# Kernel tuning notes

Measured on AMD Instinct MI355X. Metric: run time of the kernel, lower is better.

## Reference

```python
import jax, jax.numpy as jnp
import numpy as np

B = 8192
D = 512          # hidden_dim
OBS_EMB = 256
COMM = 128
N_ACT = 4
N_LAYERS = 2
D_INNER = 2 * D
D_STATE = 16
DT_RANK = D // 16  # 32
D_CONV = 4
EPS = 1e-5


def _xavier(k, shape):
    s = jnp.sqrt(2.0 / (shape[-2] + shape[-1]))
    return jax.random.normal(k, shape, jnp.float32) * s


def setup_inputs() -> dict:
    ks = jax.random.split(jax.random.key(0), 16)
    p = {}
    p['obs'] = jax.random.normal(ks[0], (B, 75), jnp.float32)
    p['comm_in'] = jax.random.normal(ks[1], (B, COMM), jnp.float32)
    # obs encoder: Conv2d(3->32, k=3, valid) + Linear(288->256)
    p['conv_w'] = jax.random.normal(ks[2], (32, 3, 3, 3), jnp.float32) * jnp.sqrt(2.0 / 27.0)
    p['conv_b'] = jnp.zeros((32,), jnp.float32)
    p['enc_w'] = _xavier(ks[3], (288, OBS_EMB))
    p['enc_b'] = jnp.zeros((OBS_EMB,), jnp.float32)
    p['proj_w'] = _xavier(ks[4], (OBS_EMB + COMM, D))
    p['proj_b'] = jnp.zeros((D,), jnp.float32)
    # Mamba stack params (stacked over layers)
    p['norm_w'] = jnp.ones((N_LAYERS, D), jnp.float32)
    p['in_proj_w'] = _xavier(ks[5], (N_LAYERS, D, 2 * D_INNER))
    p['conv1d_w'] = jax.random.normal(ks[6], (N_LAYERS, D_INNER, D_CONV), jnp.float32) / jnp.sqrt(D_CONV)
    p['conv1d_b'] = jnp.zeros((N_LAYERS, D_INNER), jnp.float32)
    p['x_proj_w'] = _xavier(ks[7], (N_LAYERS, D_INNER, DT_RANK + 2 * D_STATE))
    p['dt_proj_w'] = _xavier(ks[8], (N_LAYERS, DT_RANK, D_INNER))
    p['dt_proj_b'] = jnp.full((N_LAYERS, D_INNER), jnp.log(jnp.expm1(0.01)), jnp.float32)  # dt ~ 0.01
    p['A_log'] = jnp.log(jnp.broadcast_to(jnp.arange(1, D_STATE + 1, dtype=jnp.float32), (N_LAYERS, D_INNER, D_STATE)))
    p['D_param'] = jnp.ones((N_LAYERS, D_INNER), jnp.float32)
    p['out_proj_w'] = _xavier(ks[9], (N_LAYERS, D_INNER, D))
    p['final_norm_w'] = jnp.ones((D,), jnp.float32)
    # output heads
    p['act_w'] = _xavier(ks[10], (D, N_ACT)); p['act_b'] = jnp.zeros((N_ACT,), jnp.float32)
    p['comm_w'] = _xavier(ks[11], (D, COMM)); p['comm_b'] = jnp.zeros((COMM,), jnp.float32)
    p['val_w'] = _xavier(ks[12], (D, 1)); p['val_b'] = jnp.zeros((1,), jnp.float32)
    return p


def _rmsnorm(x, w):
    return x * jax.lax.rsqrt(jnp.mean(x * x, axis=-1, keepdims=True) + EPS) * w


def _mamba_block(u, Wi, cw, cb, Wx, Wdt, bdt, Alog, Dp, Wo):
    # u: (B, L, D) -> (B, L, D)
    Bsz, L, _ = u.shape
    d_inner = Dp.shape[0]
    x, z = jnp.split(u @ Wi, 2, axis=-1)                       # (B,L,di) each
    # causal depthwise conv1d over L
    xt = jnp.pad(jnp.swapaxes(x, 1, 2), ((0, 0), (0, 0), (D_CONV - 1, 0)))
    xc = jax.lax.conv_general_dilated(xt, cw[:, None, :], (1,), 'VALID',
                                      feature_group_count=d_inner,
                                      dimension_numbers=('NCH', 'OIH', 'NCH'))
    x = jax.nn.silu(jnp.swapaxes(xc, 1, 2) + cb)
    x_dbl = x @ Wx                                              # (B,L,dt_rank+2*ns)
    dt = jax.nn.softplus(x_dbl[..., :DT_RANK] @ Wdt + bdt)      # (B,L,di)
    Bm = x_dbl[..., DT_RANK:DT_RANK + D_STATE]                  # (B,L,ns)
    Cm = x_dbl[..., DT_RANK + D_STATE:]                         # (B,L,ns)
    A = -jnp.exp(Alog)                                          # (di,ns)
    dA = jnp.exp(dt[..., None] * A)                             # (B,L,di,ns)
    dBx = dt[..., None] * Bm[:, :, None, :] * x[..., None]      # (B,L,di,ns)

    def step(h, inp):
        dA_t, dBx_t, C_t = inp
        h = dA_t * h + dBx_t
        return h, jnp.einsum('bds,bs->bd', h, C_t)

    h0 = jnp.zeros((Bsz, d_inner, D_STATE), u.dtype)
    _, ys = jax.lax.scan(step, h0, (jnp.swapaxes(dA, 0, 1), jnp.swapaxes(dBx, 0, 1), jnp.swapaxes(Cm, 0, 1)))
    y = jnp.swapaxes(ys, 0, 1) + x * Dp
    return (y * jax.nn.silu(z)) @ Wo


def reference(obs, comm_in, conv_w, conv_b, enc_w, enc_b, proj_w, proj_b,
              norm_w, in_proj_w, conv1d_w, conv1d_b, x_proj_w, dt_proj_w, dt_proj_b,
              A_log, D_param, out_proj_w, final_norm_w,
              act_w, act_b, comm_w, comm_b, val_w, val_b):
    Bsz = obs.shape[0]
    v = obs.reshape(Bsz, 3, 5, 5)
    v = jax.lax.conv_general_dilated(v, conv_w, (1, 1), 'VALID',
                                     dimension_numbers=('NCHW', 'OIHW', 'NCHW'))
    v = jax.nn.relu(v + conv_b[None, :, None, None]).reshape(Bsz, -1)   # (B,288)
    emb = jax.nn.relu(v @ enc_w + enc_b)                                 # (B,256)
    x = jax.nn.relu(jnp.concatenate([emb, comm_in], axis=-1) @ proj_w + proj_b)  # (B,512)
    h = x[:, None, :]                                                    # (B, L=1, D)
    for i in range(norm_w.shape[0]):
        h = h + _mamba_block(_rmsnorm(h, norm_w[i]), in_proj_w[i], conv1d_w[i],
                             conv1d_b[i], x_proj_w[i], dt_proj_w[i], dt_proj_b[i],
                             A_log[i], D_param[i], out_proj_w[i])
    h = _rmsnorm(h, final_norm_w)[:, 0, :]
    action_logits = h @ act_w + act_b
    comm_out = jnp.tanh(h @ comm_w + comm_b)
    value = h @ val_w + val_b
    return action_logits, comm_out, value
```

## Files before the change

kernel.cpp:

```cpp
#include <hip/hip_runtime.h>
#include <math.h>


typedef __bf16 bf16x8 __attribute__((ext_vector_type(8)));
typedef float f32x4 __attribute__((ext_vector_type(4)));
typedef short short8 __attribute__((ext_vector_type(8)));

__device__ __forceinline__ float siluf(float v){ return v / (1.f + __expf(-v)); }
__device__ __forceinline__ float spfast(float v){ return v > 15.f ? v : __logf(1.f + __expf(v)); }
__device__ __forceinline__ float b2f(unsigned short u){ return __uint_as_float(((unsigned)u)<<16); }
__device__ __forceinline__ unsigned short f2b(float f){
  unsigned u = __float_as_uint(f);
  return (unsigned short)((u + 0x7fffu + ((u>>16)&1u)) >> 16);
}
__device__ __forceinline__ void g2l16(const void* g, void* l){
  __builtin_amdgcn_global_load_lds((const __attribute__((address_space(1))) unsigned int*)g,
                                   (__attribute__((address_space(3))) unsigned int*)l, 16, 0, 0);
}

__global__ __launch_bounds__(256) void k_wt_all(
    const float* __restrict__ in_proj_w, const float* __restrict__ out_proj_w,
    const float* __restrict__ x_proj_w,  const float* __restrict__ dt_proj_w,
    const float* __restrict__ enc_w,     const float* __restrict__ proj_w,
    const float* __restrict__ act_w, const float* __restrict__ comm_w, const float* __restrict__ val_w,
    const float* __restrict__ obs, const float* __restrict__ comm_in,
    const float* __restrict__ conv_w, const float* __restrict__ conv_b,
    unsigned short* __restrict__ wi_t, unsigned short* __restrict__ wo_t,
    unsigned short* __restrict__ wx_t, unsigned short* __restrict__ wdt_t,
    unsigned short* __restrict__ we_t, unsigned short* __restrict__ wp_t,
    unsigned short* __restrict__ wh_t,
    unsigned short* __restrict__ v, unsigned short* __restrict__ cat)
{
  int b = blockIdx.x;
  const int t = threadIdx.x;

  if (b >= 3792) {
    __shared__ float s_obs[8][76];
    const int r0 = (b - 3792) * 8;
    for (int i = t; i < 8*75; i += 256) s_obs[i/75][i%75] = obs[(size_t)(r0 + i/75)*75 + i%75];
    __syncthreads();
    for (int i = t; i < 8*288; i += 256) {
      int r = i / 288, o = i % 288;
      int c = o / 9, ij = o % 9, oi = ij/3, oj = ij%3;
      float acc = conv_b[c];
      #pragma unroll
      for (int ic=0; ic<3; ic++)
        #pragma unroll
        for (int ki=0; ki<3; ki++)
          #pragma unroll
          for (int kj=0; kj<3; kj++)
            acc = fmaf(s_obs[r][ic*25 + (oi+ki)*5 + (oj+kj)], conv_w[((c*3+ic)*3+ki)*3+kj], acc);
      v[(size_t)(r0+r)*320 + o] = f2b(fmaxf(acc, 0.f));
    }
    v[(size_t)(r0 + (t>>5))*320 + 288 + (t&31)] = 0;
    for (int i = t; i < 8*128; i += 256) {
      int r = i >> 7, c = i & 127;
      cat[(size_t)(r0+r)*384 + 256 + c] = f2b(comm_in[(size_t)(r0+r)*128 + c]);
    }
    return;
  }
  if (b >= 3536) {
    const int n = b - 3536;
    for (int k = t; k < 512; k += 256) {
      float v2;
      if (n < 4)         v2 = act_w[k*4 + n];
      else if (n < 132)  v2 = comm_w[k*128 + (n-4)];
      else if (n == 132) v2 = val_w[k];
      else               v2 = 0.f;
      wh_t[(size_t)n*512 + k] = f2b(v2);
    }
    return;
  }
  const float* Wsrc; unsigned short* Wdst; int Kd, Nd, KP, nkb;
  if (b < 2048) {
    const int L = b >> 10; b &= 1023;
    Wsrc = in_proj_w + (size_t)L*512*2048; Wdst = wi_t + (size_t)L*2048*512;
    Kd = 512; Nd = 2048; KP = 512; nkb = 16;
  } else if (b < 3072) {
    b -= 2048; const int L = b >> 9; b &= 511;
    Wsrc = out_proj_w + (size_t)L*1024*512; Wdst = wo_t + (size_t)L*512*1024;
    Kd = 1024; Nd = 512; KP = 1024; nkb = 32;
  } else if (b < 3200) {
    b -= 3072; const int L = b >> 6; b &= 63;
    Wsrc = x_proj_w + (size_t)L*1024*64; Wdst = wx_t + (size_t)L*64*1024;
    Kd = 1024; Nd = 64; KP = 1024; nkb = 32;
  } else if (b < 3264) {
    b -= 3200; const int L = b >> 5; b &= 31;
    Wsrc = dt_proj_w + (size_t)L*32*1024; Wdst = wdt_t + (size_t)L*1024*32;
    Kd = 32; Nd = 1024; KP = 32; nkb = 1;
  } else if (b < 3344) {
    b -= 3264; Wsrc = enc_w; Wdst = we_t; Kd = 288; Nd = 256; KP = 320; nkb = 10;
  } else {
    b -= 3344; Wsrc = proj_w; Wdst = wp_t; Kd = 384; Nd = 512; KP = 384; nkb = 12;
  }
  __shared__ float s[32][33];
  const int kb = (b % nkb)*32, nb = (b / nkb)*32;
  const int c = t & 31, r = t >> 5;
  #pragma unroll
  for (int i=0;i<32;i+=8) {
    const int k = kb + r + i;
    s[r+i][c] = (k < Kd) ? Wsrc[(size_t)k*Nd + nb + c] : 0.f;
  }
  __syncthreads();
  #pragma unroll
  for (int i=0;i<32;i+=8) Wdst[(size_t)(nb+r+i)*KP + kb + c] = f2b(s[c][r+i]);
}

__global__ __launch_bounds__(256) void k_rms(const float* __restrict__ h,
                                             const float* __restrict__ nw,
                                             unsigned short* __restrict__ u)
{
  const int l = threadIdx.x & 63;
  const size_t row = (size_t)blockIdx.x*4 + (threadIdx.x>>6);
  const float4* hp = (const float4*)(h + row*512) + l*2;
  float4 v0 = hp[0], v1 = hp[1];
  float ss = v0.x*v0.x+v0.y*v0.y+v0.z*v0.z+v0.w*v0.w
           + v1.x*v1.x+v1.y*v1.y+v1.z*v1.z+v1.w*v1.w;
  #pragma unroll
  for (int m=32;m;m>>=1) ss += __shfl_xor(ss, m, 64);
  const float sc = rsqrtf(ss*(1.f/512.f) + 1e-5f);
  const float4* np = (const float4*)nw + l*2;
  float4 w0 = np[0], w1 = np[1];
  short8 o;
  o[0]=(short)f2b(v0.x*sc*w0.x); o[1]=(short)f2b(v0.y*sc*w0.y);
  o[2]=(short)f2b(v0.z*sc*w0.z); o[3]=(short)f2b(v0.w*sc*w0.w);
  o[4]=(short)f2b(v1.x*sc*w1.x); o[5]=(short)f2b(v1.y*sc*w1.y);
  o[6]=(short)f2b(v1.z*sc*w1.z); o[7]=(short)f2b(v1.w*sc*w1.w);
  *(short8*)(u + row*512 + l*8) = o;
}

template<int K, int NB>
__device__ __forceinline__ void gemmT(const unsigned short* __restrict__ A,
                                      const unsigned short* __restrict__ Bt,
                                      int r0, int c0,
                                      unsigned short* sA, unsigned short* sB,
                                      f32x4 (&acc)[4][NB/32])
{
  constexpr int NF = NB/32;
  constexpr int ABUF = 128*64, BBUF = NB*64;
  const int tid = threadIdx.x;
  const int l = tid & 63;
  const int wr = (tid>>7)&1, wc = (tid>>6)&1;
  const int rowA = tid>>3, kc8 = (tid&7)*8;
  const unsigned short* gA = A  + (size_t)(r0+rowA)*K + kc8;
  const unsigned short* gB = Bt + (size_t)(c0+rowA)*K + kc8;
  const int aOff = (wr*64 + (l&15))*64 + ((l>>4)*8);
  const int bOff = (wc*(NB/2) + (l&15))*64 + ((l>>4)*8);

  auto stage = [&](int kt, int buf) {
    #pragma unroll
    for (int it=0; it<4; ++it)
      g2l16(gA + (size_t)(it*32)*K + kt, sA + buf*ABUF + (it*256+tid)*8);
    #pragma unroll
    for (int it=0; it<NF; ++it)
      g2l16(gB + (size_t)(it*32)*K + kt, sB + buf*BBUF + (it*256+tid)*8);
  };

  stage(0, 0);
  __syncthreads();
  int cur = 0;
  for (int kt=0; kt<K; kt+=64) {
    if (kt + 64 < K) stage(kt + 64, cur ^ 1);
    const unsigned short* pA = sA + cur*ABUF;
    const unsigned short* pB = sB + cur*BBUF;
    #pragma unroll
    for (int ks=0; ks<64; ks+=32) {
      bf16x8 af[4], bfm[NF];
      #pragma unroll
      for (int m=0;m<4;m++) af[m]  = *(const bf16x8*)(pA + (m*16)*64 + aOff + ks);
      #pragma unroll
      for (int n=0;n<NF;n++) bfm[n] = *(const bf16x8*)(pB + (n*16)*64 + bOff + ks);
      #pragma unroll
      for (int m=0;m<4;m++)
        #pragma unroll
        for (int n=0;n<NF;n++)
          acc[m][n] = __builtin_amdgcn_mfma_f32_16x16x32_bf16(af[m], bfm[n], acc[m][n], 0, 0, 0);
    }
    __syncthreads();
    cur ^= 1;
  }
}

__global__ __launch_bounds__(256) void k_gemm_inproj(
    const unsigned short* __restrict__ A, const unsigned short* __restrict__ Bt,
    const float* __restrict__ cw, const float* __restrict__ cb,
    unsigned short* __restrict__ xs, unsigned short* __restrict__ zs)
{
  __shared__ unsigned short sA[2*128*64], sB[2*128*64];
  f32x4 acc[4][4];
  #pragma unroll
  for (int m=0;m<4;m++)
    #pragma unroll
    for (int n=0;n<4;n++) acc[m][n] = (f32x4){0.f,0.f,0.f,0.f};
  const int r0 = blockIdx.x*128, c0 = blockIdx.y*128;
  gemmT<512,128>(A, Bt, r0, c0, sA, sB, acc);

  const int tid = threadIdx.x, l = tid & 63;
  const int wr = (tid>>7)&1, wc = (tid>>6)&1;
  const int colB = c0 + wc*64 + (l&15);
  const int rowB = r0 + wr*64 + ((l>>4)*4);
  if (c0 < 1024) {
    #pragma unroll
    for (int n=0;n<4;n++){
      const int col = colB + n*16;
      const float cw3 = cw[col*4+3], cbv = cb[col];
      #pragma unroll
      for (int m=0;m<4;m++)
        #pragma unroll
        for (int j=0;j<4;j++){
          const int row = rowB + m*16 + j;
          xs[(size_t)row*1024 + col] = f2b(siluf(fmaf(acc[m][n][j], cw3, cbv)));
        }
    }
  } else {
    #pragma unroll
    for (int n=0;n<4;n++){
      const int col = colB + n*16 - 1024;
      #pragma unroll
      for (int m=0;m<4;m++)
        #pragma unroll
        for (int j=0;j<4;j++){
          const int row = rowB + m*16 + j;
          zs[(size_t)row*1024 + col] = f2b(siluf(acc[m][n][j]));
        }
    }
  }
}

__global__ __launch_bounds__(256) void k_gemm_outproj(
    const unsigned short* __restrict__ A, const unsigned short* __restrict__ Bt,
    float* __restrict__ h)
{
  __shared__ unsigned short sA[2*128*64], sB[2*64*64];
  f32x4 acc[4][2];
  #pragma unroll
  for (int m=0;m<4;m++)
    #pragma unroll
    for (int n=0;n<2;n++) acc[m][n] = (f32x4){0.f,0.f,0.f,0.f};
  const int r0 = blockIdx.x*128, c0 = blockIdx.y*64;
  gemmT<1024,64>(A, Bt, r0, c0, sA, sB, acc);

  const int tid = threadIdx.x, l = tid & 63;
  const int wr = (tid>>7)&1, wc = (tid>>6)&1;
  const int colB = c0 + wc*32 + (l&15);
  const int rowB = r0 + wr*64 + ((l>>4)*4);
  #pragma unroll
  for (int n=0;n<2;n++){
    const int col = colB + n*16;
    #pragma unroll
    for (int m=0;m<4;m++)
      #pragma unroll
      for (int j=0;j<4;j++){
        const int row = rowB + m*16 + j;
        h[(size_t)row*512 + col] += acc[m][n][j];
      }
  }
}

__global__ __launch_bounds__(256) void k_gemm_enc(
    const unsigned short* __restrict__ A, const unsigned short* __restrict__ Bt,
    const float* __restrict__ bias, unsigned short* __restrict__ cat)
{
  __shared__ unsigned short sA[2*128*64], sB[2*64*64];
  f32x4 acc[4][2];
  #pragma unroll
  for (int m=0;m<4;m++)
    #pragma unroll
    for (int n=0;n<2;n++) acc[m][n] = (f32x4){0.f,0.f,0.f,0.f};
  const int r0 = blockIdx.x*128, c0 = blockIdx.y*64;
  gemmT<320,64>(A, Bt, r0, c0, sA, sB, acc);

  const int tid = threadIdx.x, l = tid & 63;
  const int wr = (tid>>7)&1, wc = (tid>>6)&1;
  const int colB = c0 + wc*32 + (l&15);
  const int rowB = r0 + wr*64 + ((l>>4)*4);
  #pragma unroll
  for (int n=0;n<2;n++){
    const int col = colB + n*16;
    const float bv = bias[col];
    #pragma unroll
    for (int m=0;m<4;m++)
      #pragma unroll
      for (int j=0;j<4;j++){
        const size_t row = rowB + m*16 + j;
        cat[row*384 + col] = f2b(fmaxf(acc[m][n][j] + bv, 0.f));
      }
  }
}

__global__ __launch_bounds__(256) void k_gemm_proj(
    const unsigned short* __restrict__ A, const unsigned short* __restrict__ Bt,
    const float* __restrict__ bias, float* __restrict__ h)
{
  __shared__ unsigned short sA[2*128*64], sB[2*64*64];
  f32x4 acc[4][2];
  #pragma unroll
  for (int m=0;m<4;m++)
    #pragma unroll
    for (int n=0;n<2;n++) acc[m][n] = (f32x4){0.f,0.f,0.f,0.f};
  const int r0 = blockIdx.x*128, c0 = blockIdx.y*64;
  gemmT<384,64>(A, Bt, r0, c0, sA, sB, acc);

  const int tid = threadIdx.x, l = tid & 63;
  const int wr = (tid>>7)&1, wc = (tid>>6)&1;
  const int colB = c0 + wc*32 + (l&15);
  const int rowB = r0 + wr*64 + ((l>>4)*4);
  #pragma unroll
  for (int n=0;n<2;n++){
    const int col = colB + n*16;
    const float bv = bias[col];
    #pragma unroll
    for (int m=0;m<4;m++)
      #pragma unroll
      for (int j=0;j<4;j++){
        const size_t row = rowB + m*16 + j;
        h[row*512 + col] = fmaxf(acc[m][n][j] + bv, 0.f);
      }
  }
}

__global__ __launch_bounds__(256) void k_gemm_heads(
    const unsigned short* __restrict__ A, const unsigned short* __restrict__ Bt,
    const float* __restrict__ act_b, const float* __restrict__ comm_b,
    const float* __restrict__ val_b, float* __restrict__ out)
{
  __shared__ unsigned short sA[2*128*64], sB[2*64*64];
  f32x4 acc[4][2];
  #pragma unroll
  for (int m=0;m<4;m++)
    #pragma unroll
    for (int n=0;n<2;n++) acc[m][n] = (f32x4){0.f,0.f,0.f,0.f};
  const int r0 = blockIdx.x*128, c0 = blockIdx.y*64;
  gemmT<512,64>(A, Bt, r0, c0, sA, sB, acc);

  const int tid = threadIdx.x, l = tid & 63;
  const int wr = (tid>>7)&1, wc = (tid>>6)&1;
  const int colB = c0 + wc*32 + (l&15);
  const int rowB = r0 + wr*64 + ((l>>4)*4);
  #pragma unroll
  for (int n=0;n<2;n++){
    const int col = colB + n*16;
    if (col > 132) continue;
    #pragma unroll
    for (int m=0;m<4;m++)
      #pragma unroll
      for (int j=0;j<4;j++){
        const size_t row = rowB + m*16 + j;
        float v = acc[m][n][j];
        if (col < 4)        out[row*4 + col] = v + act_b[col];
        else if (col < 132) out[32768 + row*128 + (col-4)] = tanhf(v + comm_b[col-4]);
        else                out[1081344 + row] = v + val_b[0];
      }
  }
}

__global__ __launch_bounds__(256) void k_ssm_f(
    unsigned short* __restrict__ xs, const unsigned short* __restrict__ zs,
    const unsigned short* __restrict__ Wx_t, const unsigned short* __restrict__ Wdt_t,
    const float* __restrict__ bdt, const float* __restrict__ Dp)
{
  __shared__ unsigned short sX[32*1024];
  __shared__ unsigned short sB[2*64*128];
  __shared__ float s_dbl[32][64];
  __shared__ unsigned short sDt[32*32];
  __shared__ float s_bc[32];
  constexpr int BB = 64*128;
  const int tid = threadIdx.x, l = tid & 63, w = tid >> 6;
  const int r0 = blockIdx.x * 32;

  auto stageWx = [&](int kt, int buf) {
    #pragma unroll
    for (int it=0; it<4; ++it) {
      const int idx = it*256 + tid;
      g2l16(Wx_t + (size_t)(idx>>4)*1024 + (idx&15)*8 + kt, sB + buf*BB + idx*8);
    }
  };

  #pragma unroll
  for (int it=0; it<16; ++it) {
    const int idx = it*256 + tid;
    g2l16(xs + (size_t)(r0 + (idx>>7))*1024 + (idx&127)*8, sX + idx*8);
  }
  stageWx(0, 0);
  __syncthreads();

  f32x4 acc0 = (f32x4){0.f,0.f,0.f,0.f}, acc1 = (f32x4){0.f,0.f,0.f,0.f};
  int cur = 0;
  for (int kt = 0; kt < 1024; kt += 128) {
    if (kt + 128 < 1024) stageWx(kt + 128, cur ^ 1);
    const unsigned short* pB = sB + cur*BB;
    #pragma unroll
    for (int ks=0; ks<128; ks+=32) {
      bf16x8 a0 = *(const bf16x8*)(sX + ((l&15))*1024    + (l>>4)*8 + kt + ks);
      bf16x8 a1 = *(const bf16x8*)(sX + (16+(l&15))*1024 + (l>>4)*8 + kt + ks);
      bf16x8 bf = *(const bf16x8*)(pB + (w*16+(l&15))*128 + (l>>4)*8 + ks);
      acc0 = __builtin_amdgcn_mfma_f32_16x16x32_bf16(a0, bf, acc0, 0, 0, 0);
      acc1 = __builtin_amdgcn_mfma_f32_16x16x32_bf16(a1, bf, acc1, 0, 0, 0);
    }
    __syncthreads();
    cur ^= 1;
  }

  auto stageWdt = [&](int c, int buf) {
    const int cc = c*256;
    #pragma unroll
    for (int it=0; it<4; ++it) {
      const int idx = it*256 + tid;
      g2l16(Wdt_t + (size_t)(cc + (idx>>2))*32 + (idx&3)*8, sB + buf*BB + idx*8);
    }
  };
  stageWdt(0, 0);

  #pragma unroll
  for (int j=0;j<4;j++) {
    s_dbl[(l>>4)*4 + j]     [w*16 + (l&15)] = acc0[j];
    s_dbl[16 + (l>>4)*4 + j][w*16 + (l&15)] = acc1[j];
  }
  __syncthreads();
  if (tid < 32) {
    float a = 0.f;
    #pragma unroll
    for (int s=0;s<16;s++) a = fmaf(s_dbl[tid][32+s], s_dbl[tid][48+s], a);
    s_bc[tid] = a;
  }
  {
    const int r = tid >> 3, c4 = (tid & 7)*4;
    sDt[r*32 + c4]   = f2b(s_dbl[r][c4]);
    sDt[r*32 + c4+1] = f2b(s_dbl[r][c4+1]);
    sDt[r*32 + c4+2] = f2b(s_dbl[r][c4+2]);
    sDt[r*32 + c4+3] = f2b(s_dbl[r][c4+3]);
  }
  __syncthreads();

  bf16x8 af0 = *(const bf16x8*)(sDt + ((l&15))*32    + (l>>4)*8);
  bf16x8 af1 = *(const bf16x8*)(sDt + (16+(l&15))*32 + (l>>4)*8);
  for (int c = 0; c < 4; ++c) {
    if (c + 1 < 4) stageWdt(c + 1, (c + 1) & 1);
    const unsigned short* pB = sB + (c & 1)*BB;
    f32x4 a2[2][4];
    #pragma unroll
    for (int n=0;n<4;n++){
      bf16x8 bn = *(const bf16x8*)(pB + (w*64 + n*16 + (l&15))*32 + (l>>4)*8);
      a2[0][n] = __builtin_amdgcn_mfma_f32_16x16x32_bf16(af0, bn, (f32x4){0.f,0.f,0.f,0.f}, 0, 0, 0);
      a2[1][n] = __builtin_amdgcn_mfma_f32_16x16x32_bf16(af1, bn, (f32x4){0.f,0.f,0.f,0.f}, 0, 0, 0);
    }
    const int cc = c*256;
    #pragma unroll
    for (int n=0;n<4;n++){
      const int col = cc + w*64 + n*16 + (l&15);
      const float bj = bdt[col], dpj = Dp[col];
      #pragma unroll
      for (int m=0;m<2;m++){
        #pragma unroll
        for (int j=0;j<4;j++){
          const int rloc = m*16 + (l>>4)*4 + j;
          const size_t row = r0 + rloc;
          const float dtv = spfast(a2[m][n][j] + bj);
          const float f = fmaf(dtv, s_bc[rloc], dpj);
          const float x = b2f(sX[rloc*1024 + col]);
          const float z = b2f(zs[row*1024 + col]);
          xs[row*1024 + col] = f2b(x * f * z);
        }
      }
    }
    __syncthreads();
  }
}

extern "C" void kernel_launch(void* const* d_in, const int* in_sizes, int n_in,
                              void* d_out, int out_size, void* d_ws, size_t ws_size,
                              hipStream_t stream) {
  const float* obs       = (const float*)d_in[0];
  const float* comm_in   = (const float*)d_in[1];
  const float* conv_w    = (const float*)d_in[2];
  const float* conv_b    = (const float*)d_in[3];
  const float* enc_w     = (const float*)d_in[4];
  const float* enc_b     = (const float*)d_in[5];
  const float* proj_w    = (const float*)d_in[6];
  const float* proj_b    = (const float*)d_in[7];
  const float* norm_w    = (const float*)d_in[8];
  const float* in_proj_w = (const float*)d_in[9];
  const float* conv1d_w  = (const float*)d_in[10];
  const float* conv1d_b  = (const float*)d_in[11];
  const float* x_proj_w  = (const float*)d_in[12];
  const float* dt_proj_w = (const float*)d_in[13];
  const float* dt_proj_b = (const float*)d_in[14];
  const float* D_param   = (const float*)d_in[16];
  const float* out_proj_w= (const float*)d_in[17];
  const float* final_nw  = (const float*)d_in[18];
  const float* act_w     = (const float*)d_in[19];
  const float* act_b     = (const float*)d_in[20];
  const float* comm_w    = (const float*)d_in[21];
  const float* comm_b    = (const float*)d_in[22];
  const float* val_w     = (const float*)d_in[23];
  const float* val_b     = (const float*)d_in[24];
  float* out = (float*)d_out;

  char* W = (char*)d_ws;
  float* h             = (float*)W;
  unsigned short* u_b  = (unsigned short*)(W + (16u<<20));
  unsigned short* xs_b = (unsigned short*)(W + (24u<<20));
  unsigned short* zs_b = (unsigned short*)(W + (40u<<20));
  unsigned short* wi_t = (unsigned short*)(W + (56u<<20));
  unsigned short* wo_t = (unsigned short*)(W + (60u<<20));
  unsigned short* wx_t = (unsigned short*)(W + (64u<<20));
  unsigned short* wdt_t= (unsigned short*)(W + (64u<<20) + (256u<<10));
  unsigned short* wh_t = (unsigned short*)(W + (65u<<20));
  unsigned short* we_t = (unsigned short*)(W + (65u<<20) + (512u<<10));
  unsigned short* wp_t = (unsigned short*)(W + (66u<<20));

  unsigned short* v_b   = xs_b;
  unsigned short* cat_b = zs_b;

  k_wt_all<<<4816,256,0,stream>>>(in_proj_w, out_proj_w, x_proj_w, dt_proj_w,
                                  enc_w, proj_w, act_w, comm_w, val_w,
                                  obs, comm_in, conv_w, conv_b,
                                  wi_t, wo_t, wx_t, wdt_t, we_t, wp_t, wh_t,
                                  v_b, cat_b);

  k_gemm_enc<<<dim3(64,4),256,0,stream>>>(v_b, we_t, enc_b, cat_b);
  k_gemm_proj<<<dim3(64,8),256,0,stream>>>(cat_b, wp_t, proj_b, h);

  for (int L=0; L<2; L++) {
    k_rms<<<2048,256,0,stream>>>(h, norm_w + L*512, u_b);
    k_gemm_inproj<<<dim3(64,16),256,0,stream>>>(u_b, wi_t + (size_t)L*2048*512,
                                                conv1d_w + L*1024*4, conv1d_b + L*1024, xs_b, zs_b);
    k_ssm_f<<<256,256,0,stream>>>(xs_b, zs_b, wx_t + (size_t)L*64*1024,
                                  wdt_t + (size_t)L*1024*32,
                                  dt_proj_b + L*1024, D_param + L*1024);
    k_gemm_outproj<<<dim3(64,8),256,0,stream>>>(xs_b, wo_t + (size_t)L*512*1024, h);
  }
  k_rms<<<2048,256,0,stream>>>(h, final_nw, u_b);
  k_gemm_heads<<<dim3(64,4),256,0,stream>>>(u_b, wh_t, act_b, comm_b, val_b, out);
}
```

Baseline: 235.2 us.

## Fuse RMSNorm into GEMM epilogues via row sum-of-squares and weight folding

Removes the three separate RMSNorm kernels. The norm weights are folded into the transposed in_proj and head weights. The producing GEMMs (proj, out_proj) now write a bf16 copy of h and accumulate per-row sums of squares through shared and global atomics, and the consuming GEMMs apply the rsqrt row scale in their epilogue. This saves a full read of h and a write of the normalized activations per norm, at the cost of atomics, extra zeroing blocks, and bf16 rounding of the unnormalized h before scaling.

```diff
diff --git a/kernel.cpp b/kernel.cpp
--- a/kernel.cpp
+++ b/kernel.cpp
@@ -17,23 +17,34 @@
   __builtin_amdgcn_global_load_lds((const __attribute__((address_space(1))) unsigned int*)g,
                                    (__attribute__((address_space(3))) unsigned int*)l, 16, 0, 0);
 }
+__device__ __forceinline__ float rowscale(const float* ssb, int row){
+  return rsqrtf(ssb[row]*(1.f/512.f) + 1e-5f);
+}
 
 __global__ __launch_bounds__(256) void k_wt_all(
     const float* __restrict__ in_proj_w, const float* __restrict__ out_proj_w,
     const float* __restrict__ x_proj_w,  const float* __restrict__ dt_proj_w,
     const float* __restrict__ enc_w,     const float* __restrict__ proj_w,
     const float* __restrict__ act_w, const float* __restrict__ comm_w, const float* __restrict__ val_w,
+    const float* __restrict__ norm_w, const float* __restrict__ final_nw,
     const float* __restrict__ obs, const float* __restrict__ comm_in,
     const float* __restrict__ conv_w, const float* __restrict__ conv_b,
     unsigned short* __restrict__ wi_t, unsigned short* __restrict__ wo_t,
     unsigned short* __restrict__ wx_t, unsigned short* __restrict__ wdt_t,
     unsigned short* __restrict__ we_t, unsigned short* __restrict__ wp_t,
     unsigned short* __restrict__ wh_t,
-    unsigned short* __restrict__ v, unsigned short* __restrict__ cat)
+    unsigned short* __restrict__ v, unsigned short* __restrict__ cat,
+    float* __restrict__ ssbufs )
 {
   int b = blockIdx.x;
   const int t = threadIdx.x;
 
+  if (b >= 4816) {
+    float4* p = (float4*)(ssbufs + (size_t)(b - 4816)*8192);
+    #pragma unroll
+    for (int i=0;i<8;i++) p[t + i*256] = (float4){0.f,0.f,0.f,0.f};
+    return;
+  }
   if (b >= 3792) {
     __shared__ float s_obs[8][76];
     const int r0 = (b - 3792) * 8;
@@ -67,15 +78,17 @@
       else if (n < 132)  v2 = comm_w[k*128 + (n-4)];
       else if (n == 132) v2 = val_w[k];
       else               v2 = 0.f;
-      wh_t[(size_t)n*512 + k] = f2b(v2);
+      wh_t[(size_t)n*512 + k] = f2b(v2 * final_nw[k]);
     }
     return;
   }
   const float* Wsrc; unsigned short* Wdst; int Kd, Nd, KP, nkb;
+  const float* nwf = nullptr;
   if (b < 2048) {
     const int L = b >> 10; b &= 1023;
     Wsrc = in_proj_w + (size_t)L*512*2048; Wdst = wi_t + (size_t)L*2048*512;
     Kd = 512; Nd = 2048; KP = 512; nkb = 16;
+    nwf = norm_w + L*512;
   } else if (b < 3072) {
     b -= 2048; const int L = b >> 9; b &= 511;
     Wsrc = out_proj_w + (size_t)L*1024*512; Wdst = wo_t + (size_t)L*512*1024;
@@ -102,31 +115,9 @@
     s[r+i][c] = (k < Kd) ? Wsrc[(size_t)k*Nd + nb + c] : 0.f;
   }
   __syncthreads();
-  #pragma unroll
-  for (int i=0;i<32;i+=8) Wdst[(size_t)(nb+r+i)*KP + kb + c] = f2b(s[c][r+i]);
-}
-
-__global__ __launch_bounds__(256) void k_rms(const float* __restrict__ h,
-                                             const float* __restrict__ nw,
-                                             unsigned short* __restrict__ u)
-{
-  const int l = threadIdx.x & 63;
-  const size_t row = (size_t)blockIdx.x*4 + (threadIdx.x>>6);
-  const float4* hp = (const float4*)(h + row*512) + l*2;
-  float4 v0 = hp[0], v1 = hp[1];
-  float ss = v0.x*v0.x+v0.y*v0.y+v0.z*v0.z+v0.w*v0.w
-           + v1.x*v1.x+v1.y*v1.y+v1.z*v1.z+v1.w*v1.w;
-  #pragma unroll
-  for (int m=32;m;m>>=1) ss += __shfl_xor(ss, m, 64);
-  const float sc = rsqrtf(ss*(1.f/512.f) + 1e-5f);
-  const float4* np = (const float4*)nw + l*2;
-  float4 w0 = np[0], w1 = np[1];
-  short8 o;
-  o[0]=(short)f2b(v0.x*sc*w0.x); o[1]=(short)f2b(v0.y*sc*w0.y);
-  o[2]=(short)f2b(v0.z*sc*w0.z); o[3]=(short)f2b(v0.w*sc*w0.w);
-  o[4]=(short)f2b(v1.x*sc*w1.x); o[5]=(short)f2b(v1.y*sc*w1.y);
-  o[6]=(short)f2b(v1.z*sc*w1.z); o[7]=(short)f2b(v1.w*sc*w1.w);
-  *(short8*)(u + row*512 + l*8) = o;
+  const float nwv = nwf ? nwf[kb + c] : 1.f;
+  #pragma unroll
+  for (int i=0;i<32;i+=8) Wdst[(size_t)(nb+r+i)*KP + kb + c] = f2b(s[c][r+i] * nwv);
 }
 
 template<int K, int NB>
@@ -183,6 +174,7 @@
 
 __global__ __launch_bounds__(256) void k_gemm_inproj(
     const unsigned short* __restrict__ A, const unsigned short* __restrict__ Bt,
+    const float* __restrict__ ssb,
     const float* __restrict__ cw, const float* __restrict__ cb,
     unsigned short* __restrict__ xs, unsigned short* __restrict__ zs)
 {
@@ -199,6 +191,11 @@
   const int wr = (tid>>7)&1, wc = (tid>>6)&1;
   const int colB = c0 + wc*64 + (l&15);
   const int rowB = r0 + wr*64 + ((l>>4)*4);
+  float sv[4][4];
+  #pragma unroll
+  for (int m=0;m<4;m++)
+    #pragma unroll
+    for (int j=0;j<4;j++) sv[m][j] = rowscale(ssb, rowB + m*16 + j);
   if (c0 < 1024) {
     #pragma unroll
     for (int n=0;n<4;n++){
@@ -209,7 +206,7 @@
         #pragma unroll
         for (int j=0;j<4;j++){
           const int row = rowB + m*16 + j;
-          xs[(size_t)row*1024 + col] = f2b(siluf(fmaf(acc[m][n][j], cw3, cbv)));
+          xs[(size_t)row*1024 + col] = f2b(siluf(fmaf(acc[m][n][j]*sv[m][j], cw3, cbv)));
         }
     }
   } else {
@@ -221,7 +218,7 @@
         #pragma unroll
         for (int j=0;j<4;j++){
           const int row = rowB + m*16 + j;
-          zs[(size_t)row*1024 + col] = f2b(siluf(acc[m][n][j]));
+          zs[(size_t)row*1024 + col] = f2b(siluf(acc[m][n][j]*sv[m][j]));
         }
     }
   }
@@ -229,9 +226,10 @@
 
 __global__ __launch_bounds__(256) void k_gemm_outproj(
     const unsigned short* __restrict__ A, const unsigned short* __restrict__ Bt,
-    float* __restrict__ h)
+    float* __restrict__ h, unsigned short* __restrict__ hb, float* __restrict__ ssb)
 {
   __shared__ unsigned short sA[2*128*64], sB[2*64*64];
+  __shared__ float s_ss[128];
   f32x4 acc[4][2];
   #pragma unroll
   for (int m=0;m<4;m++)
@@ -239,6 +237,45 @@
     for (int n=0;n<2;n++) acc[m][n] = (f32x4){0.f,0.f,0.f,0.f};
   const int r0 = blockIdx.x*128, c0 = blockIdx.y*64;
   gemmT<1024,64>(A, Bt, r0, c0, sA, sB, acc);
+
+  const int tid = threadIdx.x, l = tid & 63;
+  if (tid < 128) s_ss[tid] = 0.f;
+  __syncthreads();
+  const int wr = (tid>>7)&1, wc = (tid>>6)&1;
+  const int colB = c0 + wc*32 + (l&15);
+  const int rowB = r0 + wr*64 + ((l>>4)*4);
+  #pragma unroll
+  for (int m=0;m<4;m++)
+    #pragma unroll
+    for (int j=0;j<4;j++){
+      const int row = rowB + m*16 + j;
+      float c2 = 0.f;
+      #pragma unroll
+      for (int n=0;n<2;n++){
+        const int col = colB + n*16;
+        float hv = h[(size_t)row*512 + col] + acc[m][n][j];
+        h[(size_t)row*512 + col] = hv;
+        hb[(size_t)row*512 + col] = f2b(hv);
+        c2 = fmaf(hv, hv, c2);
+      }
+      atomicAdd(&s_ss[wr*64 + m*16 + ((l>>4)*4) + j], c2);
+    }
+  __syncthreads();
+  if (tid < 128) atomicAdd(&ssb[r0 + tid], s_ss[tid]);
+}
+
+__global__ __launch_bounds__(256) void k_gemm_enc(
+    const unsigned short* __restrict__ A, const unsigned short* __restrict__ Bt,
+    const float* __restrict__ bias, unsigned short* __restrict__ cat)
+{
+  __shared__ unsigned short sA[2*128*64], sB[2*64*64];
+  f32x4 acc[4][2];
+  #pragma unroll
+  for (int m=0;m<4;m++)
+    #pragma unroll
+    for (int n=0;n<2;n++) acc[m][n] = (f32x4){0.f,0.f,0.f,0.f};
+  const int r0 = blockIdx.x*128, c0 = blockIdx.y*64;
+  gemmT<320,64>(A, Bt, r0, c0, sA, sB, acc);
 
   const int tid = threadIdx.x, l = tid & 63;
   const int wr = (tid>>7)&1, wc = (tid>>6)&1;
@@ -247,19 +284,63 @@
   #pragma unroll
   for (int n=0;n<2;n++){
     const int col = colB + n*16;
+    const float bv = bias[col];
     #pragma unroll
     for (int m=0;m<4;m++)
       #pragma unroll
       for (int j=0;j<4;j++){
-        const int row = rowB + m*16 + j;
-        h[(size_t)row*512 + col] += acc[m][n][j];
+        const size_t row = rowB + m*16 + j;
+        cat[row*384 + col] = f2b(fmaxf(acc[m][n][j] + bv, 0.f));
       }
   }
 }
 
-__global__ __launch_bounds__(256) void k_gemm_enc(
+__global__ __launch_bounds__(256) void k_gemm_proj(
     const unsigned short* __restrict__ A, const unsigned short* __restrict__ Bt,
-    const float* __restrict__ bias, unsigned short* __restrict__ cat)
+    const float* __restrict__ bias, float* __restrict__ h,
+    unsigned short* __restrict__ hb, float* __restrict__ ssb)
+{
+  __shared__ unsigned short sA[2*128*64], sB[2*64*64];
+  __shared__ float s_ss[128];
+  f32x4 acc[4][2];
+  #pragma unroll
+  for (int m=0;m<4;m++)
+    #pragma unroll
+    for (int n=0;n<2;n++) acc[m][n] = (f32x4){0.f,0.f,0.f,0.f};
+  const int r0 = blockIdx.x*128, c0 = blockIdx.y*64;
+  gemmT<384,64>(A, Bt, r0, c0, sA, sB, acc);
+
+  const int tid = threadIdx.x, l = tid & 63;
+  if (tid < 128) s_ss[tid] = 0.f;
+  __syncthreads();
+  const int wr = (tid>>7)&1, wc = (tid>>6)&1;
+  const int colB = c0 + wc*32 + (l&15);
+  const int rowB = r0 + wr*64 + ((l>>4)*4);
+  #pragma unroll
+  for (int m=0;m<4;m++)
+    #pragma unroll
+    for (int j=0;j<4;j++){
+      const int row = rowB + m*16 + j;
+      float c2 = 0.f;
+      #pragma unroll
+      for (int n=0;n<2;n++){
+        const int col = colB + n*16;
+        float hv = fmaxf(acc[m][n][j] + bias[col], 0.f);
+        h[(size_t)row*512 + col] = hv;
+        hb[(size_t)row*512 + col] = f2b(hv);
+        c2 = fmaf(hv, hv, c2);
+      }
+      atomicAdd(&s_ss[wr*64 + m*16 + ((l>>4)*4) + j], c2);
+    }
+  __syncthreads();
+  if (tid < 128) atomicAdd(&ssb[r0 + tid], s_ss[tid]);
+}
+
+__global__ __launch_bounds__(256) void k_gemm_heads(
+    const unsigned short* __restrict__ A, const unsigned short* __restrict__ Bt,
+    const float* __restrict__ ssb,
+    const float* __restrict__ act_b, const float* __restrict__ comm_b,
+    const float* __restrict__ val_b, float* __restrict__ out)
 {
   __shared__ unsigned short sA[2*128*64], sB[2*64*64];
   f32x4 acc[4][2];
@@ -268,7 +349,7 @@
     #pragma unroll
     for (int n=0;n<2;n++) acc[m][n] = (f32x4){0.f,0.f,0.f,0.f};
   const int r0 = blockIdx.x*128, c0 = blockIdx.y*64;
-  gemmT<320,64>(A, Bt, r0, c0, sA, sB, acc);
+  gemmT<512,64>(A, Bt, r0, c0, sA, sB, acc);
 
   const int tid = threadIdx.x, l = tid & 63;
   const int wr = (tid>>7)&1, wc = (tid>>6)&1;
@@ -277,76 +358,13 @@
   #pragma unroll
   for (int n=0;n<2;n++){
     const int col = colB + n*16;
-    const float bv = bias[col];
+    if (col > 132) continue;
     #pragma unroll
     for (int m=0;m<4;m++)
       #pragma unroll
       for (int j=0;j<4;j++){
         const size_t row = rowB + m*16 + j;
-        cat[row*384 + col] = f2b(fmaxf(acc[m][n][j] + bv, 0.f));
-      }
-  }
-}
-
-__global__ __launch_bounds__(256) void k_gemm_proj(
-    const unsigned short* __restrict__ A, const unsigned short* __restrict__ Bt,
-    const float* __restrict__ bias, float* __restrict__ h)
-{
-  __shared__ unsigned short sA[2*128*64], sB[2*64*64];
-  f32x4 acc[4][2];
-  #pragma unroll
-  for (int m=0;m<4;m++)
-    #pragma unroll
-    for (int n=0;n<2;n++) acc[m][n] = (f32x4){0.f,0.f,0.f,0.f};
-  const int r0 = blockIdx.x*128, c0 = blockIdx.y*64;
-  gemmT<384,64>(A, Bt, r0, c0, sA, sB, acc);
-
-  const int tid = threadIdx.x, l = tid & 63;
-  const int wr = (tid>>7)&1, wc = (tid>>6)&1;
-  const int colB = c0 + wc*32 + (l&15);
-  const int rowB = r0 + wr*64 + ((l>>4)*4);
-  #pragma unroll
-  for (int n=0;n<2;n++){
-    const int col = colB + n*16;
-    const float bv = bias[col];
-    #pragma unroll
-    for (int m=0;m<4;m++)
-      #pragma unroll
-      for (int j=0;j<4;j++){
-        const size_t row = rowB + m*16 + j;
-        h[row*512 + col] = fmaxf(acc[m][n][j] + bv, 0.f);
-      }
-  }
-}
-
-__global__ __launch_bounds__(256) void k_gemm_heads(
-    const unsigned short* __restrict__ A, const unsigned short* __restrict__ Bt,
-    const float* __restrict__ act_b, const float* __restrict__ comm_b,
-    const float* __restrict__ val_b, float* __restrict__ out)
-{
-  __shared__ unsigned short sA[2*128*64], sB[2*64*64];
-  f32x4 acc[4][2];
-  #pragma unroll
-  for (int m=0;m<4;m++)
-    #pragma unroll
-    for (int n=0;n<2;n++) acc[m][n] = (f32x4){0.f,0.f,0.f,0.f};
-  const int r0 = blockIdx.x*128, c0 = blockIdx.y*64;
-  gemmT<512,64>(A, Bt, r0, c0, sA, sB, acc);
-
-  const int tid = threadIdx.x, l = tid & 63;
-  const int wr = (tid>>7)&1, wc = (tid>>6)&1;
-  const int colB = c0 + wc*32 + (l&15);
-  const int rowB = r0 + wr*64 + ((l>>4)*4);
-  #pragma unroll
-  for (int n=0;n<2;n++){
-    const int col = colB + n*16;
-    if (col > 132) continue;
-    #pragma unroll
-    for (int m=0;m<4;m++)
-      #pragma unroll
-      for (int j=0;j<4;j++){
-        const size_t row = rowB + m*16 + j;
-        float v = acc[m][n][j];
+        float v = acc[m][n][j] * rowscale(ssb, (int)row);
         if (col < 4)        out[row*4 + col] = v + act_b[col];
         else if (col < 132) out[32768 + row*128 + (col-4)] = tanhf(v + comm_b[col-4]);
         else                out[1081344 + row] = v + val_b[0];
@@ -498,11 +516,12 @@
 
   char* W = (char*)d_ws;
   float* h             = (float*)W;
-  unsigned short* u_b  = (unsigned short*)(W + (16u<<20));
+  unsigned short* hb   = (unsigned short*)(W + (16u<<20));
   unsigned short* xs_b = (unsigned short*)(W + (24u<<20));
   unsigned short* zs_b = (unsigned short*)(W + (40u<<20));
   unsigned short* wi_t = (unsigned short*)(W + (56u<<20));
   unsigned short* wo_t = (unsigned short*)(W + (60u<<20));
+  float* ssbufs        = (float*)(W + (62u<<20));
   unsigned short* wx_t = (unsigned short*)(W + (64u<<20));
   unsigned short* wdt_t= (unsigned short*)(W + (64u<<20) + (256u<<10));
   unsigned short* wh_t = (unsigned short*)(W + (65u<<20));
@@ -511,25 +530,29 @@
 
   unsigned short* v_b   = xs_b;
   unsigned short* cat_b = zs_b;
-
-  k_wt_all<<<4816,256,0,stream>>>(in_proj_w, out_proj_w, x_proj_w, dt_proj_w,
+  float* ssP = ssbufs;
+  float* ss0 = ssbufs + 8192;
+  float* ss1 = ssbufs + 16384;
+
+  k_wt_all<<<4819,256,0,stream>>>(in_proj_w, out_proj_w, x_proj_w, dt_proj_w,
                                   enc_w, proj_w, act_w, comm_w, val_w,
+                                  norm_w, final_nw,
                                   obs, comm_in, conv_w, conv_b,
                                   wi_t, wo_t, wx_t, wdt_t, we_t, wp_t, wh_t,
-                                  v_b, cat_b);
+                                  v_b, cat_b, ssbufs);
 
   k_gemm_enc<<<dim3(64,4),256,0,stream>>>(v_b, we_t, enc_b, cat_b);
-  k_gemm_proj<<<dim3(64,8),256,0,stream>>>(cat_b, wp_t, proj_b, h);
-
+  k_gemm_proj<<<dim3(64,8),256,0,stream>>>(cat_b, wp_t, proj_b, h, hb, ssP);
+
+  const float* ssin[2] = { ssP, ss0 };
+  float* ssout[2] = { ss0, ss1 };
   for (int L=0; L<2; L++) {
-    k_rms<<<2048,256,0,stream>>>(h, norm_w + L*512, u_b);
-    k_gemm_inproj<<<dim3(64,16),256,0,stream>>>(u_b, wi_t + (size_t)L*2048*512,
+    k_gemm_inproj<<<dim3(64,16),256,0,stream>>>(hb, wi_t + (size_t)L*2048*512, ssin[L],
                                                 conv1d_w + L*1024*4, conv1d_b + L*1024, xs_b, zs_b);
     k_ssm_f<<<256,256,0,stream>>>(xs_b, zs_b, wx_t + (size_t)L*64*1024,
                                   wdt_t + (size_t)L*1024*32,
                                   dt_proj_b + L*1024, D_param + L*1024);
-    k_gemm_outproj<<<dim3(64,8),256,0,stream>>>(xs_b, wo_t + (size_t)L*512*1024, h);
-  }
-  k_rms<<<2048,256,0,stream>>>(h, final_nw, u_b);
-  k_gemm_heads<<<dim3(64,4),256,0,stream>>>(u_b, wh_t, act_b, comm_b, val_b, out);
-}
+    k_gemm_outproj<<<dim3(64,8),256,0,stream>>>(xs_b, wo_t + (size_t)L*512*1024, h, hb, ssout[L]);
+  }
+  k_gemm_heads<<<dim3(64,4),256,0,stream>>>(hb, wh_t, ss1, act_b, comm_b, val_b, out);
+}
```

Measured after the change: 263.6 us. 1.12x slower.
